# Performance work log

Hardware: AMD Instinct MI355X
Metric: run time of the kernel (lower is better)

The kernel has to match this reference:

```python
import jax, jax.numpy as jnp
import numpy as np

N_EDGES = 1048576
N_CENTERS = 32768
N_SPECIES = 4
L_MAX = 3
N_BASIS = 12
N_MAX = 8
R_CUT = 5.0
NORM = 1.0 / np.sqrt(32.0)  # hypers['normalize'] = avg_num_neighbors = 32
SH_SPLITS = [0, 1, 4, 9, 16]  # cumulative offsets of (2l+1)


def real_sph_harm_lmax3(u):
    # u: [E,3] unit vectors; returns [E,16] real normalized spherical harmonics (sphericart order m=-l..l)
    x, y, z = u[:, 0], u[:, 1], u[:, 2]
    c0 = 0.5 * np.sqrt(1.0 / np.pi)
    c1 = np.sqrt(3.0 / (4.0 * np.pi))
    x2, y2, z2 = x * x, y * y, z * z
    sh = [
        jnp.full_like(x, c0),
        c1 * y, c1 * z, c1 * x,
        0.5 * np.sqrt(15.0 / np.pi) * x * y,
        0.5 * np.sqrt(15.0 / np.pi) * y * z,
        0.25 * np.sqrt(5.0 / np.pi) * (3.0 * z2 - 1.0),
        0.5 * np.sqrt(15.0 / np.pi) * x * z,
        0.25 * np.sqrt(15.0 / np.pi) * (x2 - y2),
        0.25 * np.sqrt(35.0 / (2.0 * np.pi)) * y * (3.0 * x2 - y2),
        0.5 * np.sqrt(105.0 / np.pi) * x * y * z,
        0.25 * np.sqrt(21.0 / (2.0 * np.pi)) * y * (5.0 * z2 - 1.0),
        0.25 * np.sqrt(7.0 / np.pi) * (5.0 * z2 * z - 3.0 * z),
        0.25 * np.sqrt(21.0 / (2.0 * np.pi)) * x * (5.0 * z2 - 1.0),
        0.25 * np.sqrt(105.0 / np.pi) * z * (x2 - y2),
        0.25 * np.sqrt(35.0 / (2.0 * np.pi)) * x * (x2 - y2),
    ]
    return jnp.stack(sh, axis=1)


def setup_inputs() -> dict:
    key = jax.random.key(0)
    k1, k2, k3, k4 = jax.random.split(key, 4)
    vectors = jax.random.normal(k1, (N_EDGES, 3), dtype=jnp.float32) * 1.5
    radial_weights = jax.random.normal(k2, (L_MAX + 1, N_BASIS, N_MAX), dtype=jnp.float32) * 0.1
    center_index = jax.random.randint(k3, (N_EDGES,), 0, N_CENTERS, dtype=jnp.int64)
    neighbor_species_index = jax.random.randint(k4, (N_EDGES,), 0, N_SPECIES, dtype=jnp.int64)
    return {"vectors": vectors, "radial_weights": radial_weights,
            "center_index": center_index, "neighbor_species_index": neighbor_species_index}


def reference(vectors, radial_weights, center_index, neighbor_species_index):
    # distances and unit vectors
    r = jnp.sqrt(jnp.sum(vectors * vectors, axis=-1) + 1e-12)  # [E]
    u = vectors / r[:, None]
    # smooth radial basis phi_n(r) = sin((n+1) pi r / r_cut)/r, normalized (LE-like)
    ns = jnp.arange(1, N_BASIS + 1, dtype=vectors.dtype)
    phi = jnp.sin(np.pi / R_CUT * r[:, None] * ns[None, :]) / r[:, None] * NORM  # [E, N_BASIS]
    sh = real_sph_harm_lmax3(u)  # [E,16]
    # scatter target: (center, neighbor_species) channel
    idx = center_index * N_SPECIES + neighbor_species_index  # [E]
    densities = []
    for l in range(L_MAX + 1):
        m_l = 2 * l + 1
        sh_l = jax.lax.slice_in_dim(sh, SH_SPLITS[l], SH_SPLITS[l + 1], axis=1)  # [E, 2l+1]
        rad_l = phi @ radial_weights[l]  # [E, N_MAX]
        edge_l = rad_l[:, None, :] * sh_l[:, :, None]  # [E, 2l+1, N_MAX] outer product
        dens = jax.ops.segment_sum(edge_l.reshape(edge_l.shape[0], -1), idx,
                                   num_segments=N_CENTERS * N_SPECIES)  # [N*S, m*n]
        dens = dens.reshape(N_CENTERS, N_SPECIES, m_l, N_MAX)
        dens = jnp.transpose(dens, (0, 2, 1, 3)).reshape(N_CENTERS, m_l, N_SPECIES * N_MAX)
        densities.append(dens)  # c^{a_i l}_{Ai, m, a_j n}
    # concatenate the per-l TensorMap blocks along the m axis -> [N, sum(2l+1), S*N_MAX]
    return jnp.concatenate(densities, axis=1)
```

## Files before the change

### kernel.cpp

```cpp
#include <hip/hip_runtime.h>
#include <math.h>

#define N_EDGES   1048576
#define N_SEG     131072
#define N_BUCKET  1024
#define SEG_PER_B 128
#define N_BASIS   12
#define CAP       1536

#define WS_COUNTS   0
#define WS_OFFSETS  4096
#define WS_CURSORS  8192
#define WS_SORTED   12288
#define WS_NEEDED   (12288 + 16777216)

__device__ __forceinline__ void compute_edge(float x, float y, float z,
                                             float* __restrict__ ph,
                                             float* __restrict__ sh,
                                             float& scale)
{
    const float r2    = fmaf(x, x, fmaf(y, y, z * z)) + 1e-12f;
    const float inv_r = rsqrtf(r2);
    const float r     = r2 * inv_r;
    x *= inv_r; y *= inv_r; z *= inv_r;

    const float t = 0.6283185307179586f * r;
    float s1, c1;
    __sincosf(t, &s1, &c1);
    const float twoc = 2.0f * c1;
    float skm1 = 0.0f, sk = s1;
    #pragma unroll
    for (int b = 0; b < N_BASIS; ++b) {
        ph[b] = sk;
        const float nxt = fmaf(twoc, sk, -skm1);
        skm1 = sk; sk = nxt;
    }
    scale = 0.17677669529663687f * inv_r;

    const float x2 = x * x, y2 = y * y, z2 = z * z;
    sh[0]  = 0.28209479177387814f;
    sh[1]  = 0.4886025119029199f * y;
    sh[2]  = 0.4886025119029199f * z;
    sh[3]  = 0.4886025119029199f * x;
    sh[4]  = 1.0925484305920792f * x * y;
    sh[5]  = 1.0925484305920792f * y * z;
    sh[6]  = 0.31539156525252005f * (3.0f * z2 - 1.0f);
    sh[7]  = 1.0925484305920792f * x * z;
    sh[8]  = 0.5462742152960396f * (x2 - y2);
    sh[9]  = 0.5900435899266435f * y * (3.0f * x2 - y2);
    sh[10] = 2.890611442640554f  * x * y * z;
    sh[11] = 0.4570457994644658f * y * (5.0f * z2 - 1.0f);
    sh[12] = 0.3731763325901154f * (5.0f * z2 * z - 3.0f * z);
    sh[13] = 0.4570457994644658f * x * (5.0f * z2 - 1.0f);
    sh[14] = 1.445305721320277f  * z * (x2 - y2);
    sh[15] = 0.5900435899266435f * x * (x2 - y2);
}

__global__ __launch_bounds__(256) void hist_kernel(
    const int* __restrict__ cidx, const int* __restrict__ sidx,
    int* __restrict__ counts)
{
    __shared__ int h[N_BUCKET];
    const int t = threadIdx.x;
    #pragma unroll
    for (int i = t; i < N_BUCKET; i += 256) h[i] = 0;
    __syncthreads();
    const int base = blockIdx.x * 4096;
    #pragma unroll
    for (int k = 0; k < 16; ++k) {
        const int e = base + k * 256 + t;
        const int seg = (cidx[e] << 2) | sidx[e];
        atomicAdd(&h[seg >> 7], 1);
    }
    __syncthreads();
    #pragma unroll
    for (int i = t; i < N_BUCKET; i += 256)
        if (h[i]) atomicAdd(&counts[i], h[i]);
}

__global__ __launch_bounds__(1024) void scan_kernel(
    const int* __restrict__ counts, int* __restrict__ offsets,
    int* __restrict__ cursors)
{
    __shared__ int tmp[N_BUCKET];
    const int t = threadIdx.x;
    const int orig = counts[t];
    tmp[t] = orig;
    __syncthreads();
    #pragma unroll
    for (int d = 1; d < N_BUCKET; d <<= 1) {
        const int v = (t >= d) ? tmp[t - d] : 0;
        __syncthreads();
        tmp[t] += v;
        __syncthreads();
    }
    const int off = tmp[t] - orig;
    offsets[t] = off;
    cursors[t] = off;
}

__global__ __launch_bounds__(256) void partition_kernel(
    const float* __restrict__ vectors,
    const int* __restrict__ cidx, const int* __restrict__ sidx,
    int* __restrict__ cursors, float4* __restrict__ sorted)
{
    __shared__ int bhist[N_BUCKET];
    __shared__ int bbase[N_BUCKET];
    __shared__ int lcnt[N_BUCKET];
    const int t = threadIdx.x;
    #pragma unroll
    for (int i = t; i < N_BUCKET; i += 256) bhist[i] = 0;
    __syncthreads();

    const int base = blockIdx.x * 4096;
    int segs[16];
    #pragma unroll
    for (int k = 0; k < 16; ++k) {
        const int e = base + k * 256 + t;
        segs[k] = (cidx[e] << 2) | sidx[e];
        atomicAdd(&bhist[segs[k] >> 7], 1);
    }
    __syncthreads();

    #pragma unroll
    for (int i = t; i < N_BUCKET; i += 256) {
        const int c = bhist[i];
        if (c) bbase[i] = atomicAdd(&cursors[i], c);
        lcnt[i] = 0;
    }
    __syncthreads();

    #pragma unroll
    for (int k = 0; k < 16; ++k) {
        const int e = base + k * 256 + t;
        const int seg = segs[k];
        const int bkt = seg >> 7;
        const int pos = bbase[bkt] + atomicAdd(&lcnt[bkt], 1);
        sorted[pos] = make_float4(vectors[3 * e], vectors[3 * e + 1],
                                  vectors[3 * e + 2],
                                  __int_as_float(seg & (SEG_PER_B - 1)));
    }
}

__global__ __launch_bounds__(256) void compute_kernel(
    const float4* __restrict__ sorted,
    const int* __restrict__ offsets, const int* __restrict__ counts,
    const float* __restrict__ rw,
    float* __restrict__ out)
{
    __shared__ float4 pay[CAP];
    __shared__ unsigned short ord[CAP];
    __shared__ int shist[SEG_PER_B];
    __shared__ int soff[SEG_PER_B];
    __shared__ int scur[SEG_PER_B];
    __shared__ float sW[384];

    const int t = threadIdx.x;
    const int b = blockIdx.x;
    for (int i = t; i < 384; i += 256) sW[i] = rw[i];
    if (t < SEG_PER_B) shist[t] = 0;

    const int off = offsets[b];
    const int cnt = counts[b];
    const int cntc = (cnt < CAP) ? cnt : CAP;
    __syncthreads();

    for (int i = t; i < cntc; i += 256) {
        const float4 v = sorted[off + i];
        pay[i] = v;
        atomicAdd(&shist[__float_as_int(v.w)], 1);
    }
    __syncthreads();

    if (t < SEG_PER_B) soff[t] = shist[t];
    __syncthreads();
    #pragma unroll
    for (int d = 1; d < SEG_PER_B; d <<= 1) {
        int v = 0;
        if (t >= d && t < SEG_PER_B) v = soff[t - d];
        __syncthreads();
        if (t < SEG_PER_B) soff[t] += v;
        __syncthreads();
    }
    if (t < SEG_PER_B) {
        const int ex = soff[t] - shist[t];
        soff[t] = ex;
        scur[t] = ex;
    }
    __syncthreads();

    for (int i = t; i < cntc; i += 256) {
        const int sl = __float_as_int(pay[i].w);
        const int r = atomicAdd(&scur[sl], 1);
        ord[r] = (unsigned short)i;
    }
    __syncthreads();

    const int n = t & 7;
    #pragma unroll 1
    for (int chunk = 0; chunk < 4; ++chunk) {
        const int sl = chunk * 32 + (t >> 3);
        const int js = soff[sl];
        const int je = js + shist[sl];

        float acc[16];
        #pragma unroll
        for (int L = 0; L < 16; ++L) acc[L] = 0.0f;

        for (int j = js; j < je; ++j) {
            const float4 v = pay[ord[j]];
            float ph[N_BASIS], sh[16], scale;
            compute_edge(v.x, v.y, v.z, ph, sh, scale);
            float rad[4];
            #pragma unroll
            for (int l = 0; l < 4; ++l) {
                float a = 0.0f;
                #pragma unroll
                for (int bb = 0; bb < N_BASIS; ++bb)
                    a = fmaf(ph[bb], sW[l * 96 + bb * 8 + n], a);
                rad[l] = a * scale;
            }
            #pragma unroll
            for (int L = 0; L < 16; ++L) {
                const int l = (L == 0) ? 0 : (L < 4) ? 1 : (L < 9) ? 2 : 3;
                acc[L] = fmaf(sh[L], rad[l], acc[L]);
            }
        }
        for (int j = CAP; j < cnt; ++j) {
            const float4 v = sorted[off + j];
            if (__float_as_int(v.w) != sl) continue;
            float ph[N_BASIS], sh[16], scale;
            compute_edge(v.x, v.y, v.z, ph, sh, scale);
            float rad[4];
            #pragma unroll
            for (int l = 0; l < 4; ++l) {
                float a = 0.0f;
                #pragma unroll
                for (int bb = 0; bb < N_BASIS; ++bb)
                    a = fmaf(ph[bb], sW[l * 96 + bb * 8 + n], a);
                rad[l] = a * scale;
            }
            #pragma unroll
            for (int L = 0; L < 16; ++L) {
                const int l = (L == 0) ? 0 : (L < 4) ? 1 : (L < 9) ? 2 : 3;
                acc[L] = fmaf(sh[L], rad[l], acc[L]);
            }
        }

        const int seg = b * SEG_PER_B + sl;
        float* op = out + (size_t)(seg >> 2) * 512 + (seg & 3) * 8 + n;
        #pragma unroll
        for (int L = 0; L < 16; ++L)
            op[L * 32] = acc[L];
    }
}

__global__ __launch_bounds__(256) void atomic_kernel(
    const float* __restrict__ vectors, const float* __restrict__ rw,
    const int* __restrict__ cidx, const int* __restrict__ sidx,
    float* __restrict__ out)
{
    __shared__ float sW[384];
    for (int i = threadIdx.x; i < 384; i += 256) sW[i] = rw[i];
    __syncthreads();
    const int e = blockIdx.x * 256 + threadIdx.x;
    if (e >= N_EDGES) return;
    float ph[N_BASIS], sh[16], scale;
    compute_edge(vectors[3*e], vectors[3*e+1], vectors[3*e+2], ph, sh, scale);
    float rad[4][8];
    for (int l = 0; l < 4; ++l)
        for (int n = 0; n < 8; ++n) {
            float a = 0.0f;
            for (int b = 0; b < N_BASIS; ++b)
                a = fmaf(ph[b], sW[l * 96 + b * 8 + n], a);
            rad[l][n] = a * scale;
        }
    float* op = out + (size_t)cidx[e] * 512 + sidx[e] * 8;
    for (int L = 0; L < 16; ++L) {
        const int l = (L == 0) ? 0 : (L < 4) ? 1 : (L < 9) ? 2 : 3;
        for (int n = 0; n < 8; ++n)
            atomicAdd(op + L * 32 + n, sh[L] * rad[l][n]);
    }
}

extern "C" void kernel_launch(void* const* d_in, const int* in_sizes, int n_in,
                              void* d_out, int out_size, void* d_ws, size_t ws_size,
                              hipStream_t stream) {
    const float* vectors = (const float*)d_in[0];
    const float* rw      = (const float*)d_in[1];
    const int*   cidx    = (const int*)d_in[2];
    const int*   sidx    = (const int*)d_in[3];
    float*       out     = (float*)d_out;

    if (ws_size < (size_t)WS_NEEDED) {
        hipMemsetAsync(out, 0, (size_t)out_size * sizeof(float), stream);
        hipLaunchKernelGGL(atomic_kernel, dim3(N_EDGES / 256), dim3(256), 0, stream,
                           vectors, rw, cidx, sidx, out);
        return;
    }

    char* ws = (char*)d_ws;
    int*    counts  = (int*)(ws + WS_COUNTS);
    int*    offsets = (int*)(ws + WS_OFFSETS);
    int*    cursors = (int*)(ws + WS_CURSORS);
    float4* sorted  = (float4*)(ws + WS_SORTED);

    hipMemsetAsync(counts, 0, N_BUCKET * sizeof(int), stream);

    hipLaunchKernelGGL(hist_kernel,      dim3(N_EDGES / 4096), dim3(256),  0, stream, cidx, sidx, counts);
    hipLaunchKernelGGL(scan_kernel,      dim3(1),              dim3(1024), 0, stream, counts, offsets, cursors);
    hipLaunchKernelGGL(partition_kernel, dim3(N_EDGES / 4096), dim3(256),  0, stream, vectors, cidx, sidx, cursors, sorted);
    hipLaunchKernelGGL(compute_kernel,   dim3(N_BUCKET),       dim3(256),  0, stream, sorted, offsets, counts, rw, out);
}
```

Before: 173.4 us.

## Partition packed edge indices instead of vectors; gather vectors in compute kernel

The partition pass now writes a 4-byte record (local segment id plus edge id) instead of a 16-byte float4, cutting scatter traffic and workspace size. The compute kernel loads the records, counting-sorts them in shared memory, and gathers the vectors directly into sorted order, which removes the indirect ord array. Each thread group now walks 4 contiguous segments in one pass, keeps radial weights in registers, and folds the 1/r scale into the basis values. The trade-off is random gathers of vectors inside the compute kernel and a slow fallback path for oversized buckets.

```diff
diff --git a/kernel.cpp b/kernel.cpp
--- a/kernel.cpp
+++ b/kernel.cpp
@@ -2,22 +2,20 @@
 #include <math.h>
 
 #define N_EDGES   1048576
-#define N_SEG     131072
 #define N_BUCKET  1024
 #define SEG_PER_B 128
 #define N_BASIS   12
-#define CAP       1536
+#define CAP       2048
 
 #define WS_COUNTS   0
 #define WS_OFFSETS  4096
 #define WS_CURSORS  8192
 #define WS_SORTED   12288
-#define WS_NEEDED   (12288 + 16777216)
+#define WS_NEEDED   (12288 + 4194304)
 
 __device__ __forceinline__ void compute_edge(float x, float y, float z,
                                              float* __restrict__ ph,
-                                             float* __restrict__ sh,
-                                             float& scale)
+                                             float* __restrict__ sh)
 {
     const float r2    = fmaf(x, x, fmaf(y, y, z * z)) + 1e-12f;
     const float inv_r = rsqrtf(r2);
@@ -28,14 +26,14 @@
     float s1, c1;
     __sincosf(t, &s1, &c1);
     const float twoc = 2.0f * c1;
+    const float scale = 0.17677669529663687f * inv_r;
     float skm1 = 0.0f, sk = s1;
     #pragma unroll
     for (int b = 0; b < N_BASIS; ++b) {
-        ph[b] = sk;
+        ph[b] = sk * scale;
         const float nxt = fmaf(twoc, sk, -skm1);
         skm1 = sk; sk = nxt;
     }
-    scale = 0.17677669529663687f * inv_r;
 
     const float x2 = x * x, y2 = y * y, z2 = z * z;
     sh[0]  = 0.28209479177387814f;
@@ -56,6 +54,16 @@
     sh[15] = 0.5900435899266435f * x * (x2 - y2);
 }
 
+__device__ __forceinline__ void flush_seg(const float* __restrict__ acc,
+                                          int b, int sl, int n,
+                                          float* __restrict__ out)
+{
+    const int seg = b * SEG_PER_B + sl;
+    float* op = out + (size_t)(seg >> 2) * 512 + (seg & 3) * 8 + n;
+    #pragma unroll
+    for (int L = 0; L < 16; ++L) op[L * 32] = acc[L];
+}
+
 __global__ __launch_bounds__(256) void hist_kernel(
     const int* __restrict__ cidx, const int* __restrict__ sidx,
     int* __restrict__ counts)
@@ -100,9 +108,8 @@
 }
 
 __global__ __launch_bounds__(256) void partition_kernel(
-    const float* __restrict__ vectors,
     const int* __restrict__ cidx, const int* __restrict__ sidx,
-    int* __restrict__ cursors, float4* __restrict__ sorted)
+    int* __restrict__ cursors, unsigned int* __restrict__ sorted_rec)
 {
     __shared__ int bhist[N_BUCKET];
     __shared__ int bbase[N_BUCKET];
@@ -136,39 +143,82 @@
         const int seg = segs[k];
         const int bkt = seg >> 7;
         const int pos = bbase[bkt] + atomicAdd(&lcnt[bkt], 1);
-        sorted[pos] = make_float4(vectors[3 * e], vectors[3 * e + 1],
-                                  vectors[3 * e + 2],
-                                  __int_as_float(seg & (SEG_PER_B - 1)));
+        sorted_rec[pos] = ((unsigned)(seg & 127) << 20) | (unsigned)e;
     }
 }
 
 __global__ __launch_bounds__(256) void compute_kernel(
-    const float4* __restrict__ sorted,
+    const unsigned int* __restrict__ sorted_rec,
     const int* __restrict__ offsets, const int* __restrict__ counts,
+    const float* __restrict__ vectors,
     const float* __restrict__ rw,
     float* __restrict__ out)
 {
     __shared__ float4 pay[CAP];
-    __shared__ unsigned short ord[CAP];
     __shared__ int shist[SEG_PER_B];
     __shared__ int soff[SEG_PER_B];
     __shared__ int scur[SEG_PER_B];
-    __shared__ float sW[384];
 
     const int t = threadIdx.x;
     const int b = blockIdx.x;
-    for (int i = t; i < 384; i += 256) sW[i] = rw[i];
-    if (t < SEG_PER_B) shist[t] = 0;
+    const int n = t & 7;
+    const int g = t >> 3;
+
+    float Wn[4][N_BASIS];
+    #pragma unroll
+    for (int l = 0; l < 4; ++l)
+        #pragma unroll
+        for (int bb = 0; bb < N_BASIS; ++bb)
+            Wn[l][bb] = rw[(l * N_BASIS + bb) * 8 + n];
 
     const int off = offsets[b];
     const int cnt = counts[b];
-    const int cntc = (cnt < CAP) ? cnt : CAP;
-    __syncthreads();
-
-    for (int i = t; i < cntc; i += 256) {
-        const float4 v = sorted[off + i];
-        pay[i] = v;
-        atomicAdd(&shist[__float_as_int(v.w)], 1);
+
+    if (cnt > CAP) {
+        #pragma unroll 1
+        for (int k = 0; k < 4; ++k) {
+            const int sl = g * 4 + k;
+            float acc[16];
+            #pragma unroll
+            for (int L = 0; L < 16; ++L) acc[L] = 0.0f;
+            for (int j = 0; j < cnt; ++j) {
+                const unsigned rec = sorted_rec[off + j];
+                if ((int)(rec >> 20) != sl) continue;
+                const int eid = rec & 0xFFFFF;
+                float ph[N_BASIS], sh[16];
+                compute_edge(vectors[3*eid], vectors[3*eid+1], vectors[3*eid+2], ph, sh);
+                float rad[4];
+                #pragma unroll
+                for (int l = 0; l < 4; ++l) {
+                    float a = 0.0f;
+                    #pragma unroll
+                    for (int bb = 0; bb < N_BASIS; ++bb)
+                        a = fmaf(ph[bb], Wn[l][bb], a);
+                    rad[l] = a;
+                }
+                #pragma unroll
+                for (int L = 0; L < 16; ++L) {
+                    const int l = (L == 0) ? 0 : (L < 4) ? 1 : (L < 9) ? 2 : 3;
+                    acc[L] = fmaf(sh[L], rad[l], acc[L]);
+                }
+            }
+            flush_seg(acc, b, sl, n, out);
+        }
+        return;
+    }
+
+    if (t < SEG_PER_B) shist[t] = 0;
+    __syncthreads();
+
+    unsigned recs[8];
+    const int iters = (cnt + 255) >> 8;
+    #pragma unroll
+    for (int it = 0; it < 8; ++it) {
+        const int i = it * 256 + t;
+        if (it < iters && i < cnt) {
+            recs[it] = sorted_rec[off + i];
+            atomicAdd(&shist[recs[it] >> 20], 1);
+        }
     }
     __syncthreads();
 
@@ -189,69 +239,68 @@
     }
     __syncthreads();
 
-    for (int i = t; i < cntc; i += 256) {
-        const int sl = __float_as_int(pay[i].w);
-        const int r = atomicAdd(&scur[sl], 1);
-        ord[r] = (unsigned short)i;
-    }
-    __syncthreads();
-
-    const int n = t & 7;
-    #pragma unroll 1
-    for (int chunk = 0; chunk < 4; ++chunk) {
-        const int sl = chunk * 32 + (t >> 3);
-        const int js = soff[sl];
-        const int je = js + shist[sl];
-
-        float acc[16];
+    #pragma unroll
+    for (int it = 0; it < 8; ++it) {
+        const int i = it * 256 + t;
+        if (it < iters && i < cnt) {
+            const unsigned rec = recs[it];
+            const int sl  = rec >> 20;
+            const int eid = rec & 0xFFFFF;
+            const int r = atomicAdd(&scur[sl], 1);
+            pay[r] = make_float4(vectors[3 * eid], vectors[3 * eid + 1],
+                                 vectors[3 * eid + 2], __int_as_float(sl));
+        }
+    }
+    __syncthreads();
+
+    const int s0 = g * 4;
+    const int js = soff[s0];
+    const int je = (s0 + 4 < SEG_PER_B) ? soff[s0 + 4] : cnt;
+
+    int cur = -1;
+    float acc[16];
+    #pragma unroll
+    for (int L = 0; L < 16; ++L) acc[L] = 0.0f;
+
+    for (int j = js; j < je; ++j) {
+        const float4 v = pay[j];
+        const int sl = __float_as_int(v.w);
+        if (sl != cur) {
+            if (cur >= 0) {
+                flush_seg(acc, b, cur, n, out);
+                #pragma unroll
+                for (int L = 0; L < 16; ++L) acc[L] = 0.0f;
+            }
+            cur = sl;
+        }
+        float ph[N_BASIS], sh[16];
+        compute_edge(v.x, v.y, v.z, ph, sh);
+        float rad[4];
         #pragma unroll
-        for (int L = 0; L < 16; ++L) acc[L] = 0.0f;
-
-        for (int j = js; j < je; ++j) {
-            const float4 v = pay[ord[j]];
-            float ph[N_BASIS], sh[16], scale;
-            compute_edge(v.x, v.y, v.z, ph, sh, scale);
-            float rad[4];
+        for (int l = 0; l < 4; ++l) {
+            float a = 0.0f;
             #pragma unroll
-            for (int l = 0; l < 4; ++l) {
-                float a = 0.0f;
-                #pragma unroll
-                for (int bb = 0; bb < N_BASIS; ++bb)
-                    a = fmaf(ph[bb], sW[l * 96 + bb * 8 + n], a);
-                rad[l] = a * scale;
-            }
+            for (int bb = 0; bb < N_BASIS; ++bb)
+                a = fmaf(ph[bb], Wn[l][bb], a);
+            rad[l] = a;
+        }
+        #pragma unroll
+        for (int L = 0; L < 16; ++L) {
+            const int l = (L == 0) ? 0 : (L < 4) ? 1 : (L < 9) ? 2 : 3;
+            acc[L] = fmaf(sh[L], rad[l], acc[L]);
+        }
+    }
+    if (cur >= 0) flush_seg(acc, b, cur, n, out);
+
+    #pragma unroll
+    for (int k = 0; k < 4; ++k) {
+        const int sl = s0 + k;
+        if (shist[sl] == 0) {
+            float z[16];
             #pragma unroll
-            for (int L = 0; L < 16; ++L) {
-                const int l = (L == 0) ? 0 : (L < 4) ? 1 : (L < 9) ? 2 : 3;
-                acc[L] = fmaf(sh[L], rad[l], acc[L]);
-            }
-        }
-        for (int j = CAP; j < cnt; ++j) {
-            const float4 v = sorted[off + j];
-            if (__float_as_int(v.w) != sl) continue;
-            float ph[N_BASIS], sh[16], scale;
-            compute_edge(v.x, v.y, v.z, ph, sh, scale);
-            float rad[4];
-            #pragma unroll
-            for (int l = 0; l < 4; ++l) {
-                float a = 0.0f;
-                #pragma unroll
-                for (int bb = 0; bb < N_BASIS; ++bb)
-                    a = fmaf(ph[bb], sW[l * 96 + bb * 8 + n], a);
-                rad[l] = a * scale;
-            }
-            #pragma unroll
-            for (int L = 0; L < 16; ++L) {
-                const int l = (L == 0) ? 0 : (L < 4) ? 1 : (L < 9) ? 2 : 3;
-                acc[L] = fmaf(sh[L], rad[l], acc[L]);
-            }
-        }
-
-        const int seg = b * SEG_PER_B + sl;
-        float* op = out + (size_t)(seg >> 2) * 512 + (seg & 3) * 8 + n;
-        #pragma unroll
-        for (int L = 0; L < 16; ++L)
-            op[L * 32] = acc[L];
+            for (int L = 0; L < 16; ++L) z[L] = 0.0f;
+            flush_seg(z, b, sl, n, out);
+        }
     }
 }
 
@@ -260,26 +309,21 @@
     const int* __restrict__ cidx, const int* __restrict__ sidx,
     float* __restrict__ out)
 {
-    __shared__ float sW[384];
-    for (int i = threadIdx.x; i < 384; i += 256) sW[i] = rw[i];
-    __syncthreads();
     const int e = blockIdx.x * 256 + threadIdx.x;
     if (e >= N_EDGES) return;
-    float ph[N_BASIS], sh[16], scale;
-    compute_edge(vectors[3*e], vectors[3*e+1], vectors[3*e+2], ph, sh, scale);
-    float rad[4][8];
-    for (int l = 0; l < 4; ++l)
+    float ph[N_BASIS], sh[16];
+    compute_edge(vectors[3*e], vectors[3*e+1], vectors[3*e+2], ph, sh);
+    float* op = out + (size_t)cidx[e] * 512 + sidx[e] * 8;
+    for (int l = 0; l < 4; ++l) {
+        const int L0 = l * l;
+        const int ml = 2 * l + 1;
         for (int n = 0; n < 8; ++n) {
-            float a = 0.0f;
+            float rad = 0.0f;
             for (int b = 0; b < N_BASIS; ++b)
-                a = fmaf(ph[b], sW[l * 96 + b * 8 + n], a);
-            rad[l][n] = a * scale;
-        }
-    float* op = out + (size_t)cidx[e] * 512 + sidx[e] * 8;
-    for (int L = 0; L < 16; ++L) {
-        const int l = (L == 0) ? 0 : (L < 4) ? 1 : (L < 9) ? 2 : 3;
-        for (int n = 0; n < 8; ++n)
-            atomicAdd(op + L * 32 + n, sh[L] * rad[l][n]);
+                rad = fmaf(ph[b], rw[(l * N_BASIS + b) * 8 + n], rad);
+            for (int m = 0; m < ml; ++m)
+                atomicAdd(op + (L0 + m) * 32 + n, sh[L0 + m] * rad);
+        }
     }
 }
 
@@ -300,15 +344,15 @@
     }
 
     char* ws = (char*)d_ws;
-    int*    counts  = (int*)(ws + WS_COUNTS);
-    int*    offsets = (int*)(ws + WS_OFFSETS);
-    int*    cursors = (int*)(ws + WS_CURSORS);
-    float4* sorted  = (float4*)(ws + WS_SORTED);
+    int*          counts  = (int*)(ws + WS_COUNTS);
+    int*          offsets = (int*)(ws + WS_OFFSETS);
+    int*          cursors = (int*)(ws + WS_CURSORS);
+    unsigned int* sorted  = (unsigned int*)(ws + WS_SORTED);
 
     hipMemsetAsync(counts, 0, N_BUCKET * sizeof(int), stream);
 
     hipLaunchKernelGGL(hist_kernel,      dim3(N_EDGES / 4096), dim3(256),  0, stream, cidx, sidx, counts);
     hipLaunchKernelGGL(scan_kernel,      dim3(1),              dim3(1024), 0, stream, counts, offsets, cursors);
-    hipLaunchKernelGGL(partition_kernel, dim3(N_EDGES / 4096), dim3(256),  0, stream, vectors, cidx, sidx, cursors, sorted);
-    hipLaunchKernelGGL(compute_kernel,   dim3(N_BUCKET),       dim3(256),  0, stream, sorted, offsets, counts, rw, out);
-}
+    hipLaunchKernelGGL(partition_kernel, dim3(N_EDGES / 4096), dim3(256),  0, stream, cidx, sidx, cursors, sorted);
+    hipLaunchKernelGGL(compute_kernel,   dim3(N_BUCKET),       dim3(256),  0, stream, sorted, offsets, counts, vectors, rw, out);
+}
```

After: 169.4 us. 1.02x faster.
